# Optimization experiments

Hardware: AMD Instinct MI355X
Metric: run time of the kernel (lower is better)

Reference implementation:

```python
import jax, jax.numpy as jnp
import numpy as np

DIM = 192
HEADS = 6
HEAD_DIM = DIM // HEADS
K = 3          # kernel_size
PAD = 1
STRIDE = 2
SCALE = HEAD_DIM ** -0.5
B, H, W = 16, 56, 56


def setup_inputs() -> dict:
    key = jax.random.key(0)
    ks = jax.random.split(key, 6)
    x = jax.random.normal(ks[0], (B, H, W, DIM), jnp.float32)
    # Linear weights stored as [in, out] so y = x @ W + b (== torch x @ W.T)
    Wv = jax.random.normal(ks[1], (DIM, DIM), jnp.float32) * 0.05          # v_pj, no bias
    Wa = jax.random.normal(ks[2], (DIM, K**4 * HEADS), jnp.float32) * 0.05  # attn linear
    ba = jax.random.normal(ks[3], (K**4 * HEADS,), jnp.float32) * 0.01
    Wp = jax.random.normal(ks[4], (DIM, DIM), jnp.float32) * 0.05           # proj
    bp = jax.random.normal(ks[5], (DIM,), jnp.float32) * 0.01
    return {"x": x, "Wv": Wv, "Wa": Wa, "ba": ba, "Wp": Wp, "bp": bp}


def reference(x, Wv, Wa, ba, Wp, bp):
    # Dropout layers act as identity (eval mode).
    Bn, Hn, Wn, C = x.shape
    h = -(-Hn // STRIDE)  # ceil(H/stride) = 28
    w = -(-Wn // STRIDE)
    KK = K * K

    # --- value projection + unfold (im2col over K x K window, stride STRIDE) ---
    v = x @ Wv  # [B,H,W,C]
    vp = jnp.pad(v, ((0, 0), (PAD, PAD), (PAD, PAD), (0, 0)))
    # patches: [B,h,w,K*K,C]; loop is over the fixed 3x3 kernel taps only
    patches = jnp.stack(
        [vp[:, i:i + STRIDE * h:STRIDE, j:j + STRIDE * w:STRIDE, :]
         for i in range(K) for j in range(K)], axis=3)
    patches = patches.reshape(Bn, h * w, KK, HEADS, HEAD_DIM)

    # --- attention weights from avg-pooled map (H divisible by STRIDE here) ---
    pooled = x.reshape(Bn, h, STRIDE, w, STRIDE, C).mean(axis=(2, 4))  # [B,h,w,C]
    a = pooled.reshape(Bn, h * w, C) @ Wa + ba                         # [B,hw,K^4*heads]
    a = a.reshape(Bn, h * w, HEADS, KK, KK) * SCALE
    a = jax.nn.softmax(a, axis=-1)

    # --- windowed attention: [B,hw,heads,K2,K2] x [B,hw,K2,heads,hd] ---
    out = jnp.einsum('bnhpq,bnqhd->bnphd', a, patches)  # [B,hw,K2,heads,hd]
    out = out.reshape(Bn, h, w, KK, C)

    # --- fold (scatter-add of overlapping patches back to HxW) ---
    acc = jnp.zeros((Bn, Hn + 2 * PAD, Wn + 2 * PAD, C), x.dtype)
    idx = 0
    for i in range(K):
        for j in range(K):
            acc = acc.at[:, i:i + STRIDE * h:STRIDE, j:j + STRIDE * w:STRIDE, :].add(out[:, :, :, idx, :])
            idx += 1
    y = acc[:, PAD:PAD + Hn, PAD:PAD + Wn, :]

    return y @ Wp + bp
```

## Files before the change

### kernel.cpp

```cpp
#include <hip/hip_runtime.h>
#include <cstdint>
#include <cstddef>

#define DIMC    192
#define NHEADS  6
#define NATT    486
#define NB      16
#define NH      56
#define NWW     56
#define HPOOL   28
#define WPOOL   28
#define NPIX    784
#define VH      58
#define VW      58
#define MROWS   (NB*NH*NWW)
#define MPOOL   (NB*NPIX)
#define SCALE_A 0.17677669529663687f

using bf16x8 = __attribute__((ext_vector_type(8))) short;
using f32x4  = __attribute__((ext_vector_type(4))) float;

static __device__ __forceinline__ unsigned short f2bf(float f) {
    unsigned int u = __float_as_uint(f);
    unsigned int r = (u + 0x7fffu + ((u >> 16) & 1u)) >> 16;
    return (unsigned short)r;
}
static __device__ __forceinline__ float bf2f(unsigned short u) {
    return __uint_as_float((unsigned int)u << 16);
}

__global__ __launch_bounds__(256)
void prep_kernel(const float* __restrict__ Wv, const float* __restrict__ Wp,
                 const float* __restrict__ Wa,
                 unsigned short* __restrict__ WTv, unsigned short* __restrict__ WTp,
                 unsigned short* __restrict__ WaT, unsigned int* __restrict__ vpu)
{
    int idx = blockIdx.x * 256 + threadIdx.x;
    if (idx < 73728) {
        int sel = idx / 36864;
        int r   = idx - sel * 36864;
        int n   = r / DIMC;
        int k   = r - n * DIMC;
        const float* W = sel ? Wp : Wv;
        unsigned short* WT = sel ? WTp : WTv;
        WT[r] = f2bf(W[k * DIMC + n]);
    } else if (idx < 172032) {
        int r = idx - 73728;
        int n = r / DIMC;
        int k = r - n * DIMC;
        WaT[r] = (n < NATT) ? f2bf(Wa[(size_t)k * NATT + n] * SCALE_A) : (unsigned short)0;
    } else {
        int i2   = idx - 172032;
        int cu   = i2 % 96;
        int rest = i2 / 96;
        int b    = rest / 228;
        int p    = rest - b * 228;
        int hi, wi;
        if (p < 58)       { hi = 0;  wi = p; }
        else if (p < 116) { hi = 57; wi = p - 58; }
        else { int q = p - 116; hi = 1 + (q >> 1); wi = (q & 1) * 57; }
        vpu[(((size_t)b * VH + hi) * VW + wi) * 96 + cu] = 0u;
    }
}

static __device__ __forceinline__
void gemm0_body(const float* __restrict__ x, const unsigned short* __restrict__ WT,
                unsigned short* __restrict__ vp, int by, int t, char* smem)
{
    unsigned short* As = (unsigned short*)smem;

    const int l  = t & 63;
    const int w  = t >> 6;
    const int wr = w >> 1;
    const int wc = w & 1;

    const float* Ab = x + (size_t)by * 128 * DIMC;
#pragma unroll
    for (int i = 0; i < 12; ++i) {
        int f = i * 2048 + t * 4;
        float4 v = *(const float4*)(Ab + f);
        int row = f / DIMC;
        int k   = f - row * DIMC;
        ushort4 u;
        u.x = f2bf(v.x); u.y = f2bf(v.y); u.z = f2bf(v.z); u.w = f2bf(v.w);
        int off = (row * 384 + k * 2) ^ ((row & 7) << 4);
        *(ushort4*)((char*)As + off) = u;
    }
    __syncthreads();

    f32x4 acc[2][6];
#pragma unroll
    for (int mi = 0; mi < 2; ++mi)
#pragma unroll
        for (int ni = 0; ni < 6; ++ni) acc[mi][ni] = (f32x4)0.f;

    const int arow0 = wr * 32 + (l & 15);
    const int kb    = (l >> 4) << 4;

#pragma unroll
    for (int ks = 0; ks < 6; ++ks) {
        bf16x8 a[2], b[6];
#pragma unroll
        for (int mi = 0; mi < 2; ++mi) {
            int row = arow0 + mi * 16;
            int off = (row * 384 + ks * 64 + kb) ^ ((row & 7) << 4);
            a[mi] = *(const bf16x8*)((const char*)As + off);
        }
#pragma unroll
        for (int ni = 0; ni < 6; ++ni) {
            int n = wc * 96 + ni * 16 + (l & 15);
            b[ni] = *(const bf16x8*)(WT + (size_t)n * DIMC + ks * 32 + ((l >> 4) << 3));
        }
#pragma unroll
        for (int mi = 0; mi < 2; ++mi)
#pragma unroll
            for (int ni = 0; ni < 6; ++ni)
                acc[mi][ni] = __builtin_amdgcn_mfma_f32_16x16x32_bf16(
                    a[mi], b[ni], acc[mi][ni], 0, 0, 0);
    }

    __syncthreads();
#pragma unroll
    for (int mi = 0; mi < 2; ++mi) {
#pragma unroll
        for (int r = 0; r < 4; ++r) {
            int row = wr * 32 + mi * 16 + ((l >> 4) << 2) + r;
#pragma unroll
            for (int ni = 0; ni < 6; ++ni) {
                int col = wc * 96 + ni * 16 + (l & 15);
                As[row * DIMC + col] = f2bf(acc[mi][ni][r]);
            }
        }
    }
    __syncthreads();
#pragma unroll
    for (int i = 0; i < 6; ++i) {
        int f   = i * 4096 + t * 8;
        int row = f / DIMC;
        int k   = f - row * DIMC;
        int m   = by * 128 + row;
        int bb  = m / (NH * NWW);
        int rr  = m - bb * (NH * NWW);
        int hi  = rr / NWW;
        int wi  = rr - hi * NWW;
        bf16x8 v = *(const bf16x8*)&As[f];
        unsigned short* dst = vp + (((size_t)bb * VH + hi + 1) * VW + (wi + 1)) * DIMC + k;
        *(bf16x8*)dst = v;
    }
}

static __device__ __forceinline__
void pool_body(const float* __restrict__ x, const unsigned short* __restrict__ WaT,
               const float* __restrict__ ba, unsigned short* __restrict__ attn,
               int by, int t, char* smem)
{
    unsigned short* As = (unsigned short*)smem;
    float (*Cs)[489]   = (float(*)[489])smem;
    float* ba_s        = (float*)(smem + 31296);

    const int l  = t & 63;
    const int w  = t >> 6;
    const int wr = w >> 2;
    const int wc = w & 3;

    if (t < NATT) ba_s[t] = ba[t] * SCALE_A;

#pragma unroll
    for (int i = 0; i < 6; ++i) {
        int f   = i * 2048 + t * 4;
        int row = f / DIMC;
        int k   = f - row * DIMC;
        int m   = by * 64 + row;
        int b   = m / NPIX;
        int r   = m - b * NPIX;
        int hh  = r / WPOOL;
        int ww  = r - hh * WPOOL;
        const float* xp = x + (((size_t)(b * NH + hh * 2)) * NWW + ww * 2) * DIMC + k;
        float4 v0 = *(const float4*)(xp);
        float4 v1 = *(const float4*)(xp + DIMC);
        float4 v2 = *(const float4*)(xp + (size_t)NWW * DIMC);
        float4 v3 = *(const float4*)(xp + (size_t)NWW * DIMC + DIMC);
        ushort4 u;
        u.x = f2bf(0.25f * (v0.x + v1.x + v2.x + v3.x));
        u.y = f2bf(0.25f * (v0.y + v1.y + v2.y + v3.y));
        u.z = f2bf(0.25f * (v0.z + v1.z + v2.z + v3.z));
        u.w = f2bf(0.25f * (v0.w + v1.w + v2.w + v3.w));
        int off = (row * 384 + k * 2) ^ ((row & 7) << 4);
        *(ushort4*)((char*)As + off) = u;
    }
    __syncthreads();

    f32x4 acc[2][8];
#pragma unroll
    for (int mi = 0; mi < 2; ++mi)
#pragma unroll
        for (int ni = 0; ni < 8; ++ni) acc[mi][ni] = (f32x4)0.f;

    const int arow0 = wr * 32 + (l & 15);
    const int kb    = (l >> 4) << 4;

#pragma unroll
    for (int ks = 0; ks < 6; ++ks) {
        bf16x8 a[2], b[8];
#pragma unroll
        for (int mi = 0; mi < 2; ++mi) {
            int row = arow0 + mi * 16;
            int off = (row * 384 + ks * 64 + kb) ^ ((row & 7) << 4);
            a[mi] = *(const bf16x8*)((const char*)As + off);
        }
#pragma unroll
        for (int ni = 0; ni < 8; ++ni) {
            int n = wc * 128 + ni * 16 + (l & 15);
            b[ni] = *(const bf16x8*)(WaT + (size_t)n * DIMC + ks * 32 + ((l >> 4) << 3));
        }
#pragma unroll
        for (int mi = 0; mi < 2; ++mi)
#pragma unroll
            for (int ni = 0; ni < 8; ++ni)
                acc[mi][ni] = __builtin_amdgcn_mfma_f32_16x16x32_bf16(
                    a[mi], b[ni], acc[mi][ni], 0, 0, 0);
    }

    __syncthreads();

#pragma unroll
    for (int r0 = 0; r0 < 64; r0 += 16) {
        const int mi = (r0 >> 4) & 1;
        if (wr == (r0 >> 5)) {
#pragma unroll
            for (int ni = 0; ni < 8; ++ni) {
                int col = wc * 128 + ni * 16 + (l & 15);
                if (col < NATT) {
#pragma unroll
                    for (int r = 0; r < 4; ++r)
                        Cs[((l >> 4) << 2) + r][col] =
                            (mi == 0 ? acc[0][ni][r] : acc[1][ni][r]) + ba_s[col];
                }
            }
        }
        __syncthreads();
        for (int g = t; g < 864; g += 512) {
            int lr = g / 54;
            int cg = g - lr * 54;
            const float* ap = &Cs[lr][cg * 9];
            float mx = ap[0];
#pragma unroll
            for (int q = 1; q < 9; ++q) mx = fmaxf(mx, ap[q]);
            float e[9];
            float sum = 0.f;
#pragma unroll
            for (int q = 0; q < 9; ++q) { e[q] = __expf(ap[q] - mx); sum += e[q]; }
            float inv = 1.f / sum;
            int m = by * 64 + r0 + lr;
            unsigned short* dst = attn + ((size_t)m * 54 + cg) * 16;
#pragma unroll
            for (int q = 0; q < 9; ++q) dst[q] = f2bf(e[q] * inv);
        }
        __syncthreads();
    }
}

__global__ __launch_bounds__(512)
void phase1_kernel(const float* __restrict__ x, const unsigned short* __restrict__ WTv,
                   const unsigned short* __restrict__ WaT, const float* __restrict__ ba,
                   unsigned short* __restrict__ vp, unsigned short* __restrict__ attn)
{
    __shared__ __align__(16) char smem[49152];
    const int t = threadIdx.x;
    if (blockIdx.x < 392) gemm0_body(x, WTv, vp, blockIdx.x, t, smem);
    else                  pool_body(x, WaT, ba, attn, blockIdx.x - 392, t, smem);
}

__global__ __launch_bounds__(512)
void gemm1_kernel(const unsigned short* __restrict__ Av, const unsigned short* __restrict__ WT,
                  const float* __restrict__ bias, float* __restrict__ Cv)
{
    __shared__ unsigned short As[128 * DIMC];

    const int t  = threadIdx.x;
    const int l  = t & 63;
    const int w  = t >> 6;
    const int wr = w >> 1;
    const int wc = w & 1;
    const int by = blockIdx.x;

    const unsigned short* Ab = Av + (size_t)by * 128 * DIMC;
#pragma unroll
    for (int i = 0; i < 6; ++i) {
        int f = i * 4096 + t * 8;
        bf16x8 v = *(const bf16x8*)(Ab + f);
        int row = f / DIMC;
        int k   = f - row * DIMC;
        int off = (row * 384 + k * 2) ^ ((row & 7) << 4);
        *(bf16x8*)((char*)As + off) = v;
    }
    __syncthreads();

    f32x4 acc[2][6];
#pragma unroll
    for (int mi = 0; mi < 2; ++mi)
#pragma unroll
        for (int ni = 0; ni < 6; ++ni) acc[mi][ni] = (f32x4)0.f;

    const int arow0 = wr * 32 + (l & 15);
    const int kb    = (l >> 4) << 4;

#pragma unroll
    for (int ks = 0; ks < 6; ++ks) {
        bf16x8 a[2], b[6];
#pragma unroll
        for (int mi = 0; mi < 2; ++mi) {
            int row = arow0 + mi * 16;
            int off = (row * 384 + ks * 64 + kb) ^ ((row & 7) << 4);
            a[mi] = *(const bf16x8*)((const char*)As + off);
        }
#pragma unroll
        for (int ni = 0; ni < 6; ++ni) {
            int n = wc * 96 + ni * 16 + (l & 15);
            b[ni] = *(const bf16x8*)(WT + (size_t)n * DIMC + ks * 32 + ((l >> 4) << 3));
        }
#pragma unroll
        for (int mi = 0; mi < 2; ++mi)
#pragma unroll
            for (int ni = 0; ni < 6; ++ni)
                acc[mi][ni] = __builtin_amdgcn_mfma_f32_16x16x32_bf16(
                    a[mi], b[ni], acc[mi][ni], 0, 0, 0);
    }

    float* fAs = (float*)As;
#pragma unroll
    for (int chunk = 0; chunk < 4; ++chunk) {
        __syncthreads();
        if (wr == chunk) {
#pragma unroll
            for (int mi = 0; mi < 2; ++mi) {
#pragma unroll
                for (int r = 0; r < 4; ++r) {
                    int rowl = mi * 16 + ((l >> 4) << 2) + r;
#pragma unroll
                    for (int ni = 0; ni < 6; ++ni) {
                        int col = wc * 96 + ni * 16 + (l & 15);
                        fAs[rowl * DIMC + col] = acc[mi][ni][r];
                    }
                }
            }
        }
        __syncthreads();
#pragma unroll
        for (int i = 0; i < 3; ++i) {
            int f   = i * 2048 + t * 4;
            int row = f / DIMC;
            int k   = f - row * DIMC;
            int m   = by * 128 + chunk * 32 + row;
            float4 v  = *(const float4*)&fAs[f];
            float4 bv = *(const float4*)&bias[k];
            v.x += bv.x; v.y += bv.y; v.z += bv.z; v.w += bv.w;
            *(float4*)(Cv + (size_t)m * DIMC + k) = v;
        }
    }
}

template<int NI, int NJ>
static __device__ __forceinline__ void gather_body(
    int b, int p, int qc, int head, int c,
    const unsigned short* __restrict__ attn, const unsigned short* __restrict__ vp,
    unsigned short* __restrict__ y)
{
    const int pr = p >> 1;
    const int qr = qc >> 1;

    bf16x8        aw8[NI * NJ];
    unsigned short aw9[NI * NJ];
    ushort2       v[NI * NJ][9];
    bool          ok[NI * NJ];

#pragma unroll
    for (int wi = 0; wi < NI; ++wi) {
        const bool hv  = (NI == 1) || (wi == 0) || (pr + 1 < HPOOL);
        const int  hhs = hv ? (pr + wi) : (HPOOL - 1);
        const int  iof = (NI == 1) ? 1 : (wi ? 0 : 2);
#pragma unroll
        for (int wj = 0; wj < NJ; ++wj) {
            const bool wv  = (NJ == 1) || (wj == 0) || (qr + 1 < WPOOL);
            const int  wws = wv ? (qr + wj) : (WPOOL - 1);
            const int  jof = (NJ == 1) ? 1 : (wj ? 0 : 2);
            const int  idx = wi * NJ + wj;
            ok[idx] = hv && wv;

            const unsigned short* ap = attn +
                ((size_t)((b * NPIX + hhs * WPOOL + wws) * 54 + head * 9 + iof * 3 + jof)) * 16;
            aw8[idx] = *(const bf16x8*)ap;
            aw9[idx] = ap[8];

            const unsigned short* vb = vp +
                (((size_t)(b * VH + 2 * hhs)) * VW + 2 * wws) * DIMC + c;
#pragma unroll
            for (int qi = 0; qi < 3; ++qi)
#pragma unroll
                for (int qj = 0; qj < 3; ++qj)
                    v[idx][qi * 3 + qj] = *(const ushort2*)(vb + ((size_t)qi * VW + qj) * DIMC);
        }
    }

    float accx = 0.f, accy = 0.f;
#pragma unroll
    for (int idx = 0; idx < NI * NJ; ++idx) {
#pragma unroll
        for (int k = 0; k < 9; ++k) {
            float a = ok[idx]
                ? ((k < 8) ? bf2f((unsigned short)aw8[idx][k]) : bf2f(aw9[idx]))
                : 0.f;
            accx = fmaf(a, bf2f(v[idx][k].x), accx);
            accy = fmaf(a, bf2f(v[idx][k].y), accy);
        }
    }

    size_t pix = (size_t)b * (NH * NWW) + (size_t)p * NWW + qc;
    ushort2 r;
    r.x = f2bf(accx);
    r.y = f2bf(accy);
    *(ushort2*)(y + pix * DIMC + c) = r;
}

__global__ __launch_bounds__(192)
void gather_kernel(const unsigned short* __restrict__ attn,
                   const unsigned short* __restrict__ vp,
                   unsigned short* __restrict__ y)
{
    const int t    = threadIdx.x;
    const int pl   = t / 96;
    const int c2   = t - pl * 96;
    const int c    = c2 * 2;
    const int head = c2 >> 4;

    const int flat = blockIdx.x;
    const int wgid = (flat & 7) * 3136 + (flat >> 3);
    const int b    = wgid / 1568;
    const int rr   = wgid - b * 1568;
    const int p    = rr / 28;
    const int wq   = rr - p * 28;
    const int qc   = wq + pl * 28;

    if (p & 1) {
        if (wq & 1) gather_body<2, 2>(b, p, qc, head, c, attn, vp, y);
        else        gather_body<2, 1>(b, p, qc, head, c, attn, vp, y);
    } else {
        if (wq & 1) gather_body<1, 2>(b, p, qc, head, c, attn, vp, y);
        else        gather_body<1, 1>(b, p, qc, head, c, attn, vp, y);
    }
}

extern "C" void kernel_launch(void* const* d_in, const int* in_sizes, int n_in,
                              void* d_out, int out_size, void* d_ws, size_t ws_size,
                              hipStream_t stream)
{
    const float* x  = (const float*)d_in[0];
    const float* Wv = (const float*)d_in[1];
    const float* Wa = (const float*)d_in[2];
    const float* ba = (const float*)d_in[3];
    const float* Wp = (const float*)d_in[4];
    const float* bp = (const float*)d_in[5];
    float* out = (float*)d_out;

    const size_t vp_elems   = (size_t)NB * VH * VW * DIMC;
    const size_t attn_elems = (size_t)MPOOL * 54 * 16;
    const size_t y_elems    = (size_t)MROWS * DIMC;

    unsigned short* vp   = (unsigned short*)d_ws;
    unsigned short* attn = vp + vp_elems;
    unsigned short* y    = attn + attn_elems;
    unsigned short* WTv  = y + y_elems;
    unsigned short* WTp  = WTv + 36864;
    unsigned short* WaT  = WTp + 36864;

    prep_kernel<<<2040, 256, 0, stream>>>(Wv, Wp, Wa, WTv, WTp, WaT, (unsigned int*)vp);

    phase1_kernel<<<588, 512, 0, stream>>>(x, WTv, WaT, ba, vp, attn);

    gather_kernel<<<25088, 192, 0, stream>>>(attn, vp, y);

    gemm1_kernel<<<MROWS / 128, 512, 0, stream>>>(y, WTp, bp, out);
}
```

Before: 114.1 us.

## Pre-convert x to bf16 in prep and stage GEMM tiles with async global-to-LDS loads

The fp32-to-bf16 conversion of x moves out of the GEMM0 tile load and into prep_kernel, which writes a bf16 copy of x to the workspace. Both GEMM kernels then fill their swizzled LDS A tiles with global_load_lds 16-byte direct copies, applying the XOR swizzle on the source address instead of going through registers. This costs an extra full pass over x (fp32 read plus bf16 write) in prep, but GEMM0 reads half the bytes and register staging is avoided. The pool path still reads fp32 x.

```diff
diff --git a/kernel.cpp b/kernel.cpp
--- a/kernel.cpp
+++ b/kernel.cpp
@@ -15,6 +15,7 @@
 #define VW      58
 #define MROWS   (NB*NH*NWW)
 #define MPOOL   (NB*NPIX)
+#define XELEMS  (MROWS*DIMC)
 #define SCALE_A 0.17677669529663687f
 
 using bf16x8 = __attribute__((ext_vector_type(8))) short;
@@ -29,11 +30,18 @@
     return __uint_as_float((unsigned int)u << 16);
 }
 
+static __device__ __forceinline__ void gload_lds16(const void* src, void* lds) {
+    __builtin_amdgcn_global_load_lds(
+        (const __attribute__((address_space(1))) void*)src,
+        (__attribute__((address_space(3))) void*)lds, 16, 0, 0);
+}
+
 __global__ __launch_bounds__(256)
 void prep_kernel(const float* __restrict__ Wv, const float* __restrict__ Wp,
-                 const float* __restrict__ Wa,
+                 const float* __restrict__ Wa, const float* __restrict__ x,
                  unsigned short* __restrict__ WTv, unsigned short* __restrict__ WTp,
-                 unsigned short* __restrict__ WaT, unsigned int* __restrict__ vpu)
+                 unsigned short* __restrict__ WaT, unsigned int* __restrict__ vpu,
+                 unsigned short* __restrict__ xb)
 {
     int idx = blockIdx.x * 256 + threadIdx.x;
     if (idx < 73728) {
@@ -49,7 +57,7 @@
         int n = r / DIMC;
         int k = r - n * DIMC;
         WaT[r] = (n < NATT) ? f2bf(Wa[(size_t)k * NATT + n] * SCALE_A) : (unsigned short)0;
-    } else {
+    } else if (idx < 522240) {
         int i2   = idx - 172032;
         int cu   = i2 % 96;
         int rest = i2 / 96;
@@ -60,11 +68,35 @@
         else if (p < 116) { hi = 57; wi = p - 58; }
         else { int q = p - 116; hi = 1 + (q >> 1); wi = (q & 1) * 57; }
         vpu[(((size_t)b * VH + hi) * VW + wi) * 96 + cu] = 0u;
+    } else {
+        size_t xi = (size_t)(idx - 522240) * 8;
+        float4 v0 = *(const float4*)(x + xi);
+        float4 v1 = *(const float4*)(x + xi + 4);
+        bf16x8 u;
+        u[0] = (short)f2bf(v0.x); u[1] = (short)f2bf(v0.y);
+        u[2] = (short)f2bf(v0.z); u[3] = (short)f2bf(v0.w);
+        u[4] = (short)f2bf(v1.x); u[5] = (short)f2bf(v1.y);
+        u[6] = (short)f2bf(v1.z); u[7] = (short)f2bf(v1.w);
+        *(bf16x8*)(xb + xi) = u;
     }
 }
 
 static __device__ __forceinline__
-void gemm0_body(const float* __restrict__ x, const unsigned short* __restrict__ WT,
+void stage_tile_async(const unsigned short* __restrict__ Ab, unsigned short* As, int t)
+{
+#pragma unroll
+    for (int i = 0; i < 6; ++i) {
+        int L     = i * 8192 + t * 16;
+        int row   = L / 384;
+        int inrow = L - row * 384;
+        int s     = (row & 7) << 4;
+        const unsigned short* src = Ab + (size_t)row * DIMC + ((inrow ^ s) >> 1);
+        gload_lds16(src, (char*)As + i * 8192 + (t >> 6) * 1024);
+    }
+}
+
+static __device__ __forceinline__
+void gemm0_body(const unsigned short* __restrict__ xb, const unsigned short* __restrict__ WT,
                 unsigned short* __restrict__ vp, int by, int t, char* smem)
 {
     unsigned short* As = (unsigned short*)smem;
@@ -74,18 +106,7 @@
     const int wr = w >> 1;
     const int wc = w & 1;
 
-    const float* Ab = x + (size_t)by * 128 * DIMC;
-#pragma unroll
-    for (int i = 0; i < 12; ++i) {
-        int f = i * 2048 + t * 4;
-        float4 v = *(const float4*)(Ab + f);
-        int row = f / DIMC;
-        int k   = f - row * DIMC;
-        ushort4 u;
-        u.x = f2bf(v.x); u.y = f2bf(v.y); u.z = f2bf(v.z); u.w = f2bf(v.w);
-        int off = (row * 384 + k * 2) ^ ((row & 7) << 4);
-        *(ushort4*)((char*)As + off) = u;
-    }
+    stage_tile_async(xb + (size_t)by * 128 * DIMC, As, t);
     __syncthreads();
 
     f32x4 acc[2][6];
@@ -261,13 +282,14 @@
 }
 
 __global__ __launch_bounds__(512)
-void phase1_kernel(const float* __restrict__ x, const unsigned short* __restrict__ WTv,
+void phase1_kernel(const unsigned short* __restrict__ xb, const float* __restrict__ x,
+                   const unsigned short* __restrict__ WTv,
                    const unsigned short* __restrict__ WaT, const float* __restrict__ ba,
                    unsigned short* __restrict__ vp, unsigned short* __restrict__ attn)
 {
     __shared__ __align__(16) char smem[49152];
     const int t = threadIdx.x;
-    if (blockIdx.x < 392) gemm0_body(x, WTv, vp, blockIdx.x, t, smem);
+    if (blockIdx.x < 392) gemm0_body(xb, WTv, vp, blockIdx.x, t, smem);
     else                  pool_body(x, WaT, ba, attn, blockIdx.x - 392, t, smem);
 }
 
@@ -275,7 +297,7 @@
 void gemm1_kernel(const unsigned short* __restrict__ Av, const unsigned short* __restrict__ WT,
                   const float* __restrict__ bias, float* __restrict__ Cv)
 {
-    __shared__ unsigned short As[128 * DIMC];
+    __shared__ __align__(16) unsigned short As[128 * DIMC];
 
     const int t  = threadIdx.x;
     const int l  = t & 63;
@@ -284,16 +306,7 @@
     const int wc = w & 1;
     const int by = blockIdx.x;
 
-    const unsigned short* Ab = Av + (size_t)by * 128 * DIMC;
-#pragma unroll
-    for (int i = 0; i < 6; ++i) {
-        int f = i * 4096 + t * 8;
-        bf16x8 v = *(const bf16x8*)(Ab + f);
-        int row = f / DIMC;
-        int k   = f - row * DIMC;
-        int off = (row * 384 + k * 2) ^ ((row & 7) << 4);
-        *(bf16x8*)((char*)As + off) = v;
-    }
+    stage_tile_async(Av + (size_t)by * 128 * DIMC, As, t);
     __syncthreads();
 
     f32x4 acc[2][6];
@@ -472,10 +485,12 @@
     unsigned short* WTv  = y + y_elems;
     unsigned short* WTp  = WTv + 36864;
     unsigned short* WaT  = WTp + 36864;
-
-    prep_kernel<<<2040, 256, 0, stream>>>(Wv, Wp, Wa, WTv, WTp, WaT, (unsigned int*)vp);
-
-    phase1_kernel<<<588, 512, 0, stream>>>(x, WTv, WaT, ba, vp, attn);
+    unsigned short* xb   = WaT + 98304;
+
+    prep_kernel<<<6744, 256, 0, stream>>>(Wv, Wp, Wa, x, WTv, WTp, WaT,
+                                          (unsigned int*)vp, xb);
+
+    phase1_kernel<<<588, 512, 0, stream>>>(xb, x, WTv, WaT, ba, vp, attn);
 
     gather_kernel<<<25088, 192, 0, stream>>>(attn, vp, y);
 
```

After: 115.9 us. Within noise of the previous version (+1.6%).
